# Kernel tuning notes

Measured on AMD Instinct MI355X. Metric: run time of the kernel, lower is better.

Reference implementation:

```python
import jax, jax.numpy as jnp
import numpy as np

B, C, H, W = 2, 256, 128, 128
O = 256          # out_channels
KH = KW = 3
K = KH * KW      # 9 kernel taps
PAD, DIL = 1, 1


def setup_inputs() -> dict:
    key = jax.random.key(0)
    k1, k2, k3, k4, k5 = jax.random.split(key, 5)
    x = jax.random.normal(k1, (B, C, H, W), dtype=jnp.float32)
    # offset/mask predicting conv: 3*groups*K = 27 output channels.
    # scaled small so predicted offsets are O(1) pixels (torch inits these to 0).
    w_off = jax.random.normal(k2, (3 * K, C, KH, KW), dtype=jnp.float32) * 0.01
    b_off = jax.random.normal(k3, (3 * K,), dtype=jnp.float32) * 0.01
    # main weight is 1x1, later tiled to 3x3 (weight.repeat([1,1,3,3]))
    stdv = 1.0 / np.sqrt(C * KH * KW)
    weight = jax.random.uniform(k4, (O, C, 1, 1), dtype=jnp.float32, minval=-stdv, maxval=stdv)
    bias = jax.random.normal(k5, (O,), dtype=jnp.float32) * 0.01
    return {"x": x, "w_off": w_off, "b_off": b_off, "weight": weight, "bias": bias}


def _bilinear_gather(img, py, px):
    # img: [C,H,W]; py/px: [K,H,W] float sample coords. Zero outside bounds.
    y0 = jnp.floor(py).astype(jnp.int32)
    x0 = jnp.floor(px).astype(jnp.int32)
    ly = py - y0
    lx = px - x0

    def corner(yc, xc):
        valid = (yc >= 0) & (yc < H) & (xc >= 0) & (xc < W)
        v = img[:, jnp.clip(yc, 0, H - 1), jnp.clip(xc, 0, W - 1)]  # [C,K,H,W]
        return jnp.where(valid[None], v, 0.0)

    return (corner(y0, x0) * ((1 - ly) * (1 - lx))[None]
            + corner(y0, x0 + 1) * ((1 - ly) * lx)[None]
            + corner(y0 + 1, x0) * (ly * (1 - lx))[None]
            + corner(y0 + 1, x0 + 1) * (ly * lx)[None])


def reference(x, w_off, b_off, weight, bias):
    # --- offset/mask prediction conv (3x3, pad 1) ---
    tmp = jax.lax.conv_general_dilated(
        x, w_off, window_strides=(1, 1), padding=((PAD, PAD), (PAD, PAD)),
        rhs_dilation=(DIL, DIL), dimension_numbers=("NCHW", "OIHW", "NCHW"))
    tmp = tmp + b_off[None, :, None, None]
    o1, o2, mask = tmp[:, :K], tmp[:, K:2 * K], tmp[:, 2 * K:]
    offset = jnp.concatenate([o1, o2], axis=1)          # [B, 2K, H, W]
    dy = offset[:, 0::2]                                # [B, K, H, W]
    dx = offset[:, 1::2]
    # softmax over the SPATIAL axis per mask channel (as in the source)
    mask = jax.nn.softmax(mask.reshape(B, K, H * W), axis=2).reshape(B, K, H, W)

    # --- sampling grid ---
    kk = jnp.arange(K)
    ki = (kk // KW).astype(jnp.float32)
    kj = (kk % KW).astype(jnp.float32)
    base_y = ki[:, None, None] * DIL - PAD + jnp.arange(H, dtype=jnp.float32)[None, :, None]
    base_x = kj[:, None, None] * DIL - PAD + jnp.arange(W, dtype=jnp.float32)[None, None, :]
    py = dy + base_y[None]                              # [B, K, H, W]
    px = dx + base_x[None]

    sampled = jax.vmap(_bilinear_gather)(x, py, px)     # [B, C, K, H, W]
    sampled = sampled * mask[:, None]                   # modulated

    # weight.repeat([1,1,3,3]) -> same 1x1 weight at every tap
    Wk = jnp.tile(weight, (1, 1, KH, KW)).reshape(O, C, K)
    out = jnp.einsum("bckhw,ock->bohw", sampled, Wk) + bias[None, :, None, None]
    return out
```

## Files before the change

### kernel.cpp

```cpp
#include <hip/hip_runtime.h>
#include <hip/hip_fp16.h>

#define Bx 2
#define Cx 256
#define Hx 128
#define Wx 128
#define HWx (Hx*Wx)
#define Ox 256
#define Kx 9
#define NOFF 27
#define KK 2304

typedef __attribute__((ext_vector_type(8))) _Float16 f16x8;
typedef __attribute__((ext_vector_type(4))) float f32x4;


__device__ __forceinline__ unsigned short f2h(float f) {
    return __half_as_ushort(__float2half_rn(f));
}

__global__ void k_prep(const float* __restrict__ w_off, const float* __restrict__ weight,
                       unsigned short* __restrict__ wb, unsigned short* __restrict__ wq) {
    int i = blockIdx.x * 256 + threadIdx.x;
    if (i < 32 * KK) {
        int oc = i / KK;
        int k  = i - oc * KK;
        int tap = k >> 8;
        int c   = k & 255;
        float v = (oc < NOFF) ? w_off[(oc * Cx + c) * 9 + tap] : 0.f;
        wb[i] = f2h(v);
    } else {
        int j = i - 32 * KK;
        if (j < Ox * Cx) wq[j] = f2h(weight[j]);
    }
}

__global__ __launch_bounds__(256) void k_tr(
        const float* __restrict__ x, unsigned short* __restrict__ xtb) {
    __shared__ float tl[64][65];
    int tid = threadIdx.x;
    int hw0 = blockIdx.x * 64;
    int c0  = blockIdx.y * 64;
    int b   = blockIdx.z;
#pragma unroll
    for (int r = 0; r < 4; r++) {
        int cl = r * 16 + (tid >> 4);
        int hl = (tid & 15) * 4;
        const float4 v = *(const float4*)&x[((size_t)(b * Cx + c0 + cl)) * HWx + hw0 + hl];
        tl[cl][hl + 0] = v.x; tl[cl][hl + 1] = v.y; tl[cl][hl + 2] = v.z; tl[cl][hl + 3] = v.w;
    }
    __syncthreads();
#pragma unroll
    for (int r = 0; r < 4; r++) {
        int hl = r * 16 + (tid >> 4);
        int cl = (tid & 15) * 4;
        ushort4 o;
        o.x = f2h(tl[cl + 0][hl]); o.y = f2h(tl[cl + 1][hl]);
        o.z = f2h(tl[cl + 2][hl]); o.w = f2h(tl[cl + 3][hl]);
        *(ushort4*)&xtb[((size_t)b * HWx + hw0 + hl) * Cx + c0 + cl] = o;
    }
}

__global__ __launch_bounds__(256) void k1_mfma(
        const unsigned short* __restrict__ xtb, const unsigned short* __restrict__ wb,
        const float* __restrict__ b_off, float* __restrict__ tmp_t) {
    int band = blockIdx.x & 7;
    int sub  = blockIdx.x >> 3;
    int y    = band * 16 + sub;
    int b    = blockIdx.y;

    __shared__ unsigned short As[390 * 72];
    int tid  = threadIdx.x;
    int wave = tid >> 6, lane = tid & 63;
    int quad = lane >> 4, col = lane & 15;

    f32x4 acc[2][2] = {};
    const unsigned short* xb = xtb + (size_t)b * HWx * Cx;

#pragma unroll 1
    for (int ph = 0; ph < 4; ph++) {
        __syncthreads();
        for (int u = tid; u < 3120; u += 256) {
            int slot = u >> 3;
            int ci   = (u & 7) * 8;
            int r = (slot >= 260) ? 2 : (slot >= 130 ? 1 : 0);
            int p = slot - r * 130;
            int yy = y + r - 1;
            int px = p - 1;
            uint4 v = make_uint4(0u, 0u, 0u, 0u);
            if (yy >= 0 && yy < Hx && px >= 0 && px < Wx)
                v = *(const uint4*)(xb + ((size_t)(yy * Wx + px)) * Cx + ph * 64 + ci);
            *(uint4*)&As[slot * 72 + ci] = v;
        }
        __syncthreads();
#pragma unroll
        for (int r = 0; r < 3; r++)
#pragma unroll
        for (int dc = 0; dc < 3; dc++)
#pragma unroll
        for (int s = 0; s < 2; s++) {
            int kl  = s * 32 + quad * 8;
            int tap = r * 3 + dc;
            int kg  = tap * 256 + ph * 64 + kl;
            int base = r * 130 + dc;
            f16x8 a0 = *(const f16x8*)&As[(base + wave * 32 + col) * 72 + kl];
            f16x8 a1 = *(const f16x8*)&As[(base + wave * 32 + 16 + col) * 72 + kl];
            f16x8 b0 = *(const f16x8*)(wb + (size_t)col * KK + kg);
            f16x8 b1 = *(const f16x8*)(wb + (size_t)(16 + col) * KK + kg);
            acc[0][0] = __builtin_amdgcn_mfma_f32_16x16x32_f16(a0, b0, acc[0][0], 0, 0, 0);
            acc[0][1] = __builtin_amdgcn_mfma_f32_16x16x32_f16(a0, b1, acc[0][1], 0, 0, 0);
            acc[1][0] = __builtin_amdgcn_mfma_f32_16x16x32_f16(a1, b0, acc[1][0], 0, 0, 0);
            acc[1][1] = __builtin_amdgcn_mfma_f32_16x16x32_f16(a1, b1, acc[1][1], 0, 0, 0);
        }
    }

    float* orow = tmp_t + ((size_t)(b * HWx) + (size_t)y * Wx) * 32;
#pragma unroll
    for (int nt = 0; nt < 2; nt++) {
        int oc = nt * 16 + col;
        float bo = (oc < NOFF) ? b_off[oc] : 0.f;
#pragma unroll
        for (int mt = 0; mt < 2; mt++)
#pragma unroll
            for (int r4 = 0; r4 < 4; r4++) {
                int pxd = wave * 32 + mt * 16 + quad * 4 + r4;
                orow[(size_t)pxd * 32 + oc] = acc[mt][nt][r4] + bo;
            }
    }
}

__global__ __launch_bounds__(256) void k2a(
        const float* __restrict__ tmp_t, float* __restrict__ pscr) {
    int b  = blockIdx.y;
    int hw = blockIdx.x * 256 + threadIdx.x;
    const float* row = tmp_t + ((size_t)b * HWx + hw) * 32;
    float4 v0 = *(const float4*)(row + 16);
    float4 v1 = *(const float4*)(row + 20);
    float4 v2 = *(const float4*)(row + 24);
    float lv[9] = {v0.z, v0.w, v1.x, v1.y, v1.z, v1.w, v2.x, v2.y, v2.z};

    __shared__ float wm[4][9], wsum[4][9];
    int tid = threadIdx.x;
    int wave = tid >> 6, lane = tid & 63;

    float mx[9];
#pragma unroll
    for (int k = 0; k < 9; k++) mx[k] = lv[k];
    for (int off = 32; off > 0; off >>= 1)
#pragma unroll
        for (int k = 0; k < 9; k++) mx[k] = fmaxf(mx[k], __shfl_down(mx[k], off));
    if (lane == 0)
#pragma unroll
        for (int k = 0; k < 9; k++) wm[wave][k] = mx[k];
    __syncthreads();
    float M[9];
#pragma unroll
    for (int k = 0; k < 9; k++)
        M[k] = fmaxf(fmaxf(wm[0][k], wm[1][k]), fmaxf(wm[2][k], wm[3][k]));
    float sm[9];
#pragma unroll
    for (int k = 0; k < 9; k++) sm[k] = __expf(lv[k] - M[k]);
    for (int off = 32; off > 0; off >>= 1)
#pragma unroll
        for (int k = 0; k < 9; k++) sm[k] += __shfl_down(sm[k], off);
    if (lane == 0)
#pragma unroll
        for (int k = 0; k < 9; k++) wsum[wave][k] = sm[k];
    __syncthreads();
    if (tid < 9) {
        float S = wsum[0][tid] + wsum[1][tid] + wsum[2][tid] + wsum[3][tid];
        int idx = (b * 64 + blockIdx.x) * 9 + tid;
        pscr[idx] = M[tid];
        pscr[1152 + idx] = S;
    }
}

__global__ void k2b(const float* __restrict__ pscr, float* __restrict__ stats) {
    int bk = blockIdx.x;
    int b = bk / Kx, k = bk % Kx;
    int s = threadIdx.x;
    int idx = (b * 64 + s) * 9 + k;
    float m = pscr[idx];
    float p = pscr[1152 + idx];
    float M = m;
    for (int off = 32; off > 0; off >>= 1) M = fmaxf(M, __shfl_down(M, off));
    M = __shfl(M, 0);
    float e = p * __expf(m - M);
    for (int off = 32; off > 0; off >>= 1) e += __shfl_down(e, off);
    if (s == 0) { stats[bk * 2] = M; stats[bk * 2 + 1] = 1.f / e; }
}

__global__ __launch_bounds__(256) void k35_fused(
        const unsigned short* __restrict__ xtb, const float* __restrict__ tmp_t,
        const float* __restrict__ stats, const unsigned short* __restrict__ wq,
        const float* __restrict__ bias, float* __restrict__ out) {
    __shared__ __half2 lwh[64][36];
    __shared__ int     lo[64][36];
    __shared__ unsigned short As[64][264];
    int tid  = threadIdx.x;
    int band = blockIdx.x & 7;
    int sub  = blockIdx.x >> 3;
    int b    = blockIdx.y;
    int px0  = (band * 32 + sub) * 64;

    for (int u = tid; u < 576; u += 256) {
        int px = u / 9, k = u - px * 9;
        int hw = px0 + px;
        int y  = hw >> 7;
        int xx = hw & (Wx - 1);
        const float* trow = tmp_t + ((size_t)b * HWx + hw) * 32;
        float dy = trow[2 * k];
        float dx = trow[2 * k + 1];
        float lg = trow[18 + k];
        float m  = __expf(lg - stats[(b * Kx + k) * 2]) * stats[(b * Kx + k) * 2 + 1] * 256.f;
        float py = dy + (float)(k / 3 - 1 + y);
        float px_ = dx + (float)(k % 3 - 1 + xx);
        float fy = floorf(py), fx = floorf(px_);
        int y0 = (int)fy, x0 = (int)fx;
        float ly = py - fy, lx = px_ - fx;
        float w00 = (1.f - ly) * (1.f - lx) * m;
        float w01 = (1.f - ly) * lx * m;
        float w10 = ly * (1.f - lx) * m;
        float w11 = ly * lx * m;
        int y1 = y0 + 1, x1 = x0 + 1;
        bool vy0 = (y0 >= 0) & (y0 < Hx), vy1 = (y1 >= 0) & (y1 < Hx);
        bool vx0 = (x0 >= 0) & (x0 < Wx), vx1 = (x1 >= 0) & (x1 < Wx);
        int cy0 = min(max(y0, 0), Hx - 1), cy1 = min(max(y1, 0), Hx - 1);
        int cx0 = min(max(x0, 0), Wx - 1), cx1 = min(max(x1, 0), Wx - 1);
        float a00 = (vy0 && vx0) ? w00 : 0.f;
        float a01 = (vy0 && vx1) ? w01 : 0.f;
        float a10 = (vy1 && vx0) ? w10 : 0.f;
        float a11 = (vy1 && vx1) ? w11 : 0.f;
        lwh[px][4 * k + 0] = __half2half2(__float2half_rn(a00));  lo[px][4 * k + 0] = cy0 * Wx + cx0;
        lwh[px][4 * k + 1] = __half2half2(__float2half_rn(a01));  lo[px][4 * k + 1] = cy0 * Wx + cx1;
        lwh[px][4 * k + 2] = __half2half2(__float2half_rn(a10));  lo[px][4 * k + 2] = cy1 * Wx + cx0;
        lwh[px][4 * k + 3] = __half2half2(__float2half_rn(a11));  lo[px][4 * k + 3] = cy1 * Wx + cx1;
    }
    __syncthreads();

    int wave = tid >> 6;
    int lane = tid & 63;
    int half = lane >> 5;
    int li   = lane & 31;
    const unsigned short* xb = xtb + (size_t)b * HWx * Cx + li * 8;
    const __half2 uns = __half2half2(__float2half_rn(1.f / 256.f));
#pragma unroll 1
    for (int pass = 0; pass < 8; pass++) {
        int px = wave * 16 + pass * 2 + half;
        __half2 a0 = __half2half2(__ushort_as_half(0));
        __half2 a1 = a0, a2 = a0, a3 = a0;
#pragma unroll
        for (int j = 0; j < 36; j++) {
            __half2 w = lwh[px][j];
            int   off = lo[px][j];
            uint4 v = *(const uint4*)(xb + (size_t)off * Cx);
            a0 = __hfma2(w, *(__half2*)&v.x, a0);
            a1 = __hfma2(w, *(__half2*)&v.y, a1);
            a2 = __hfma2(w, *(__half2*)&v.z, a2);
            a3 = __hfma2(w, *(__half2*)&v.w, a3);
        }
        a0 = __hmul2(a0, uns); a1 = __hmul2(a1, uns);
        a2 = __hmul2(a2, uns); a3 = __hmul2(a3, uns);
        uint4 r;
        r.x = *(unsigned*)&a0; r.y = *(unsigned*)&a1;
        r.z = *(unsigned*)&a2; r.w = *(unsigned*)&a3;
        *(uint4*)&As[px][li * 8] = r;
    }
    __syncthreads();

    int quad = lane >> 4, col = lane & 15;
    f32x4 acc[4][4] = {};
#pragma unroll
    for (int ki = 0; ki < 8; ki++) {
        int k0 = ki * 32;
        f16x8 a[4], w[4];
#pragma unroll
        for (int mt = 0; mt < 4; mt++)
            a[mt] = *(const f16x8*)&As[mt * 16 + col][k0 + quad * 8];
#pragma unroll
        for (int nt = 0; nt < 4; nt++)
            w[nt] = *(const f16x8*)(wq + (size_t)(wave * 64 + nt * 16 + col) * Cx + k0 + quad * 8);
#pragma unroll
        for (int mt = 0; mt < 4; mt++)
#pragma unroll
            for (int nt = 0; nt < 4; nt++)
                acc[mt][nt] = __builtin_amdgcn_mfma_f32_16x16x32_f16(a[mt], w[nt], acc[mt][nt], 0, 0, 0);
    }

#pragma unroll
    for (int nt = 0; nt < 4; nt++) {
        int oc = wave * 64 + nt * 16 + col;
        float bo = bias[oc];
#pragma unroll
        for (int mt = 0; mt < 4; mt++) {
            int hw = px0 + mt * 16 + quad * 4;
            float4 v;
            v.x = acc[mt][nt][0] + bo; v.y = acc[mt][nt][1] + bo;
            v.z = acc[mt][nt][2] + bo; v.w = acc[mt][nt][3] + bo;
            *(float4*)&out[((size_t)(b * Ox + oc)) * HWx + hw] = v;
        }
    }
}

extern "C" void kernel_launch(void* const* d_in, const int* in_sizes, int n_in,
                              void* d_out, int out_size, void* d_ws, size_t ws_size,
                              hipStream_t stream) {
    const float*    x      = (const float*)d_in[0];
    const float*    w_off  = (const float*)d_in[1];
    const float*    b_off  = (const float*)d_in[2];
    const float*    weight = (const float*)d_in[3];
    const float*    bias   = (const float*)d_in[4];
    float* out = (float*)d_out;
    float* ws  = (float*)d_ws;

    float*          tmp_t = ws;
    float*          pscr  = ws + 1048576;
    float*          stats = ws + 1050880;
    unsigned short* wbq   = (unsigned short*)(ws + 1050944);
    unsigned short* xtb   = (unsigned short*)(ws + 1087808);
    unsigned short* wq    = (unsigned short*)(ws + 5282112);

    k_prep<<<dim3(544), 256, 0, stream>>>(w_off, weight, wbq, wq);
    k_tr<<<dim3(HWx / 64, Cx / 64, Bx), 256, 0, stream>>>(x, xtb);
    k1_mfma<<<dim3(128, Bx), 256, 0, stream>>>(xtb, wbq, b_off, tmp_t);
    k2a<<<dim3(64, Bx), 256, 0, stream>>>(tmp_t, pscr);
    k2b<<<dim3(Bx * Kx), 64, 0, stream>>>(pscr, stats);
    k35_fused<<<dim3(256, Bx), 256, 0, stream>>>(xtb, tmp_t, stats, wq, bias, out);
}
```

Measured before the change: 169.1 us.

## Fuse prep with transpose, fold softmax partials into offset conv, halve conv tiles

Merges the weight-prep and x-transpose kernels into one launch. The offset-conv kernel now handles half-row tiles of 64 pixels, doubling its grid to 512 blocks, and computes per-block softmax max and sum partials straight from its accumulators, which removes the separate k2a pass that re-read tmp_t. k2b now reduces 256 partials per channel with 4 waves. The intent is fewer launches, better CU occupancy in the conv, and one less global read of tmp_t. The cost is redundant halo loads for the smaller tiles and fewer MFMAs per B-operand load.

```diff
diff --git a/kernel.cpp b/kernel.cpp
--- a/kernel.cpp
+++ b/kernel.cpp
@@ -19,29 +19,33 @@
     return __half_as_ushort(__float2half_rn(f));
 }
 
-__global__ void k_prep(const float* __restrict__ w_off, const float* __restrict__ weight,
-                       unsigned short* __restrict__ wb, unsigned short* __restrict__ wq) {
-    int i = blockIdx.x * 256 + threadIdx.x;
-    if (i < 32 * KK) {
-        int oc = i / KK;
-        int k  = i - oc * KK;
-        int tap = k >> 8;
-        int c   = k & 255;
-        float v = (oc < NOFF) ? w_off[(oc * Cx + c) * 9 + tap] : 0.f;
-        wb[i] = f2h(v);
-    } else {
-        int j = i - 32 * KK;
-        if (j < Ox * Cx) wq[j] = f2h(weight[j]);
-    }
-}
-
-__global__ __launch_bounds__(256) void k_tr(
-        const float* __restrict__ x, unsigned short* __restrict__ xtb) {
+__global__ __launch_bounds__(256) void k_pt(
+        const float* __restrict__ x, const float* __restrict__ w_off,
+        const float* __restrict__ weight,
+        unsigned short* __restrict__ xtb, unsigned short* __restrict__ wb,
+        unsigned short* __restrict__ wq) {
+    if (blockIdx.x >= 2048) {
+        int i = (blockIdx.x - 2048) * 256 + threadIdx.x;
+        if (i < 32 * KK) {
+            int oc = i / KK;
+            int k  = i - oc * KK;
+            int tap = k >> 8;
+            int c   = k & 255;
+            float v = (oc < NOFF) ? w_off[(oc * Cx + c) * 9 + tap] : 0.f;
+            wb[i] = f2h(v);
+        } else {
+            int j = i - 32 * KK;
+            if (j < Ox * Cx) wq[j] = f2h(weight[j]);
+        }
+        return;
+    }
     __shared__ float tl[64][65];
     int tid = threadIdx.x;
-    int hw0 = blockIdx.x * 64;
-    int c0  = blockIdx.y * 64;
-    int b   = blockIdx.z;
+    int t   = blockIdx.x;
+    int b   = t >> 10;
+    int r2  = t & 1023;
+    int hw0 = (r2 >> 2) * 64;
+    int c0  = (r2 & 3) * 64;
 #pragma unroll
     for (int r = 0; r < 4; r++) {
         int cl = r * 16 + (tid >> 4);
@@ -63,30 +67,34 @@
 
 __global__ __launch_bounds__(256) void k1_mfma(
         const unsigned short* __restrict__ xtb, const unsigned short* __restrict__ wb,
-        const float* __restrict__ b_off, float* __restrict__ tmp_t) {
+        const float* __restrict__ b_off, float* __restrict__ tmp_t,
+        float* __restrict__ pscr) {
     int band = blockIdx.x & 7;
-    int sub  = blockIdx.x >> 3;
-    int y    = band * 16 + sub;
+    int idx  = blockIdx.x >> 3;
+    int y    = band * 16 + (idx >> 1);
+    int hf   = idx & 1;
+    int px0  = hf * 64;
     int b    = blockIdx.y;
 
-    __shared__ unsigned short As[390 * 72];
+    __shared__ unsigned short As[198 * 72];
+    __shared__ float wm[4][9], wsum[4][9];
     int tid  = threadIdx.x;
     int wave = tid >> 6, lane = tid & 63;
     int quad = lane >> 4, col = lane & 15;
 
-    f32x4 acc[2][2] = {};
+    f32x4 acc[2] = {};
     const unsigned short* xb = xtb + (size_t)b * HWx * Cx;
 
 #pragma unroll 1
     for (int ph = 0; ph < 4; ph++) {
         __syncthreads();
-        for (int u = tid; u < 3120; u += 256) {
+        for (int u = tid; u < 1584; u += 256) {
             int slot = u >> 3;
             int ci   = (u & 7) * 8;
-            int r = (slot >= 260) ? 2 : (slot >= 130 ? 1 : 0);
-            int p = slot - r * 130;
+            int r = (slot >= 132) ? 2 : (slot >= 66 ? 1 : 0);
+            int p = slot - r * 66;
             int yy = y + r - 1;
-            int px = p - 1;
+            int px = px0 + p - 1;
             uint4 v = make_uint4(0u, 0u, 0u, 0u);
             if (yy >= 0 && yy < Hx && px >= 0 && px < Wx)
                 v = *(const uint4*)(xb + ((size_t)(yy * Wx + px)) * Cx + ph * 64 + ci);
@@ -102,76 +110,51 @@
             int kl  = s * 32 + quad * 8;
             int tap = r * 3 + dc;
             int kg  = tap * 256 + ph * 64 + kl;
-            int base = r * 130 + dc;
-            f16x8 a0 = *(const f16x8*)&As[(base + wave * 32 + col) * 72 + kl];
-            f16x8 a1 = *(const f16x8*)&As[(base + wave * 32 + 16 + col) * 72 + kl];
+            int base = r * 66 + dc;
+            f16x8 a0 = *(const f16x8*)&As[(base + wave * 16 + col) * 72 + kl];
             f16x8 b0 = *(const f16x8*)(wb + (size_t)col * KK + kg);
             f16x8 b1 = *(const f16x8*)(wb + (size_t)(16 + col) * KK + kg);
-            acc[0][0] = __builtin_amdgcn_mfma_f32_16x16x32_f16(a0, b0, acc[0][0], 0, 0, 0);
-            acc[0][1] = __builtin_amdgcn_mfma_f32_16x16x32_f16(a0, b1, acc[0][1], 0, 0, 0);
-            acc[1][0] = __builtin_amdgcn_mfma_f32_16x16x32_f16(a1, b0, acc[1][0], 0, 0, 0);
-            acc[1][1] = __builtin_amdgcn_mfma_f32_16x16x32_f16(a1, b1, acc[1][1], 0, 0, 0);
-        }
-    }
-
-    float* orow = tmp_t + ((size_t)(b * HWx) + (size_t)y * Wx) * 32;
+            acc[0] = __builtin_amdgcn_mfma_f32_16x16x32_f16(a0, b0, acc[0], 0, 0, 0);
+            acc[1] = __builtin_amdgcn_mfma_f32_16x16x32_f16(a0, b1, acc[1], 0, 0, 0);
+        }
+    }
+
+    float* orow = tmp_t + ((size_t)(b * HWx) + (size_t)y * Wx + px0) * 32;
 #pragma unroll
     for (int nt = 0; nt < 2; nt++) {
         int oc = nt * 16 + col;
         float bo = (oc < NOFF) ? b_off[oc] : 0.f;
 #pragma unroll
-        for (int mt = 0; mt < 2; mt++)
-#pragma unroll
-            for (int r4 = 0; r4 < 4; r4++) {
-                int pxd = wave * 32 + mt * 16 + quad * 4 + r4;
-                orow[(size_t)pxd * 32 + oc] = acc[mt][nt][r4] + bo;
-            }
-    }
-}
-
-__global__ __launch_bounds__(256) void k2a(
-        const float* __restrict__ tmp_t, float* __restrict__ pscr) {
-    int b  = blockIdx.y;
-    int hw = blockIdx.x * 256 + threadIdx.x;
-    const float* row = tmp_t + ((size_t)b * HWx + hw) * 32;
-    float4 v0 = *(const float4*)(row + 16);
-    float4 v1 = *(const float4*)(row + 20);
-    float4 v2 = *(const float4*)(row + 24);
-    float lv[9] = {v0.z, v0.w, v1.x, v1.y, v1.z, v1.w, v2.x, v2.y, v2.z};
-
-    __shared__ float wm[4][9], wsum[4][9];
-    int tid = threadIdx.x;
-    int wave = tid >> 6, lane = tid & 63;
-
-    float mx[9];
-#pragma unroll
-    for (int k = 0; k < 9; k++) mx[k] = lv[k];
-    for (int off = 32; off > 0; off >>= 1)
-#pragma unroll
-        for (int k = 0; k < 9; k++) mx[k] = fmaxf(mx[k], __shfl_down(mx[k], off));
-    if (lane == 0)
-#pragma unroll
-        for (int k = 0; k < 9; k++) wm[wave][k] = mx[k];
-    __syncthreads();
-    float M[9];
-#pragma unroll
-    for (int k = 0; k < 9; k++)
-        M[k] = fmaxf(fmaxf(wm[0][k], wm[1][k]), fmaxf(wm[2][k], wm[3][k]));
-    float sm[9];
-#pragma unroll
-    for (int k = 0; k < 9; k++) sm[k] = __expf(lv[k] - M[k]);
-    for (int off = 32; off > 0; off >>= 1)
-#pragma unroll
-        for (int k = 0; k < 9; k++) sm[k] += __shfl_down(sm[k], off);
-    if (lane == 0)
-#pragma unroll
-        for (int k = 0; k < 9; k++) wsum[wave][k] = sm[k];
+        for (int r4 = 0; r4 < 4; r4++) {
+            int pxd = wave * 16 + quad * 4 + r4;
+            float v = acc[nt][r4] + bo;
+            acc[nt][r4] = v;
+            orow[(size_t)pxd * 32 + oc] = v;
+        }
+    }
+
+    float m4 = fmaxf(fmaxf(acc[1][0], acc[1][1]), fmaxf(acc[1][2], acc[1][3]));
+    m4 = fmaxf(m4, __shfl_xor(m4, 16));
+    m4 = fmaxf(m4, __shfl_xor(m4, 32));
+    float s4 = __expf(acc[1][0] - m4) + __expf(acc[1][1] - m4)
+             + __expf(acc[1][2] - m4) + __expf(acc[1][3] - m4);
+    s4 += __shfl_xor(s4, 16);
+    s4 += __shfl_xor(s4, 32);
+    if (quad == 0 && col >= 2 && col <= 10) {
+        wm[wave][col - 2] = m4;
+        wsum[wave][col - 2] = s4;
+    }
     __syncthreads();
     if (tid < 9) {
-        float S = wsum[0][tid] + wsum[1][tid] + wsum[2][tid] + wsum[3][tid];
-        int idx = (b * 64 + blockIdx.x) * 9 + tid;
-        pscr[idx] = M[tid];
-        pscr[1152 + idx] = S;
+        float M = fmaxf(fmaxf(wm[0][tid], wm[1][tid]), fmaxf(wm[2][tid], wm[3][tid]));
+        float S = wsum[0][tid] * __expf(wm[0][tid] - M)
+                + wsum[1][tid] * __expf(wm[1][tid] - M)
+                + wsum[2][tid] * __expf(wm[2][tid] - M)
+                + wsum[3][tid] * __expf(wm[3][tid] - M);
+        int blkid = y * 2 + hf;
+        int pidx  = (b * 256 + blkid) * 9 + tid;
+        pscr[pidx] = M;
+        pscr[4608 + pidx] = S;
     }
 }
 
@@ -179,15 +162,24 @@
     int bk = blockIdx.x;
     int b = bk / Kx, k = bk % Kx;
     int s = threadIdx.x;
-    int idx = (b * 64 + s) * 9 + k;
+    int idx = (b * 256 + s) * 9 + k;
     float m = pscr[idx];
-    float p = pscr[1152 + idx];
+    float p = pscr[4608 + idx];
     float M = m;
-    for (int off = 32; off > 0; off >>= 1) M = fmaxf(M, __shfl_down(M, off));
-    M = __shfl(M, 0);
+    for (int off = 32; off > 0; off >>= 1) M = fmaxf(M, __shfl_xor(M, off));
     float e = p * __expf(m - M);
-    for (int off = 32; off > 0; off >>= 1) e += __shfl_down(e, off);
-    if (s == 0) { stats[bk * 2] = M; stats[bk * 2 + 1] = 1.f / e; }
+    for (int off = 32; off > 0; off >>= 1) e += __shfl_xor(e, off);
+    __shared__ float sm[4], ss[4];
+    int wave = s >> 6, lane = s & 63;
+    if (lane == 0) { sm[wave] = M; ss[wave] = e; }
+    __syncthreads();
+    if (s == 0) {
+        float Mf = fmaxf(fmaxf(sm[0], sm[1]), fmaxf(sm[2], sm[3]));
+        float S = ss[0] * __expf(sm[0] - Mf) + ss[1] * __expf(sm[1] - Mf)
+                + ss[2] * __expf(sm[2] - Mf) + ss[3] * __expf(sm[3] - Mf);
+        stats[bk * 2] = Mf;
+        stats[bk * 2 + 1] = 1.f / S;
+    }
 }
 
 __global__ __launch_bounds__(256) void k35_fused(
@@ -315,15 +307,13 @@
 
     float*          tmp_t = ws;
     float*          pscr  = ws + 1048576;
-    float*          stats = ws + 1050880;
-    unsigned short* wbq   = (unsigned short*)(ws + 1050944);
-    unsigned short* xtb   = (unsigned short*)(ws + 1087808);
-    unsigned short* wq    = (unsigned short*)(ws + 5282112);
-
-    k_prep<<<dim3(544), 256, 0, stream>>>(w_off, weight, wbq, wq);
-    k_tr<<<dim3(HWx / 64, Cx / 64, Bx), 256, 0, stream>>>(x, xtb);
-    k1_mfma<<<dim3(128, Bx), 256, 0, stream>>>(xtb, wbq, b_off, tmp_t);
-    k2a<<<dim3(64, Bx), 256, 0, stream>>>(tmp_t, pscr);
-    k2b<<<dim3(Bx * Kx), 64, 0, stream>>>(pscr, stats);
+    float*          stats = ws + 1057792;
+    unsigned short* wbq   = (unsigned short*)(ws + 1057856);
+    unsigned short* xtb   = (unsigned short*)(ws + 1076288);
+    unsigned short* wq    = (unsigned short*)(ws + 5270592);
+
+    k_pt<<<dim3(2592), 256, 0, stream>>>(x, w_off, weight, xtb, wbq, wq);
+    k1_mfma<<<dim3(256, Bx), 256, 0, stream>>>(xtb, wbq, b_off, tmp_t, pscr);
+    k2b<<<dim3(Bx * Kx), 256, 0, stream>>>(pscr, stats);
     k35_fused<<<dim3(256, Bx), 256, 0, stream>>>(xtb, tmp_t, stats, wq, bias, out);
 }
```

Measured after the change: 167.8 us. Within noise of the previous version (-0.8%).
